# Performance work log

Hardware: AMD Instinct MI355X
Metric: run time of the kernel (lower is better)

Reference implementation:

```python
import jax, jax.numpy as jnp
import numpy as np

P_SIZE = 5
NUM_HEAD = 8
GN_EPS = 1e-5
LRELU_SLOPE = 0.2


def conv1x1(w, x, b=None):
    # w: [out_c, in_c], x: [n, in_c, h, w]
    y = jnp.einsum('oc,nchw->nohw', w, x)
    if b is not None:
        y = y + b[None, :, None, None]
    return y


def bilinear_sample(feat, sx, sy):
    """grid_sample(mode='bilinear', padding_mode='zeros', align_corners=True).
    With align_corners=True the normalize/denormalize round-trip in
    deformation_grid/grid_sample is the identity, so sx,sy are raw pixel coords.
    feat: [n,c,H,W]; sx,sy: [n,P,H,W] -> out [n,c,P,H,W]."""
    n, c, H, W = feat.shape
    x0 = jnp.floor(sx)
    y0 = jnp.floor(sy)
    x1 = x0 + 1.0
    y1 = y0 + 1.0
    wx1 = sx - x0
    wx0 = 1.0 - wx1
    wy1 = sy - y0
    wy0 = 1.0 - wy1
    feat_flat = feat.reshape(n, c, H * W)

    def corner(xi, yi, wgt):
        valid = (xi >= 0) & (xi <= W - 1) & (yi >= 0) & (yi <= H - 1)
        xc = jnp.clip(xi, 0, W - 1).astype(jnp.int32)
        yc = jnp.clip(yi, 0, H - 1).astype(jnp.int32)
        idx = (yc * W + xc).reshape(n, -1)                      # [n, P*H*W]
        g = jnp.take_along_axis(feat_flat, idx[:, None, :], axis=2)  # [n,c,P*H*W]
        g = g.reshape(n, c, xi.shape[1], H, W)                  # [n,c,P,H,W]
        wm = (wgt * valid.astype(feat.dtype))[:, None]          # [n,1,P,H,W]
        return g * wm

    return (corner(x0, y0, wx0 * wy0) + corner(x1, y0, wx1 * wy0)
            + corner(x0, y1, wx0 * wy1) + corner(x1, y1, wx1 * wy1))


def sample_coords(deform_field, p_size):
    # deform_field: [n,2,h,w] -> absolute pixel coords sx, sy: [n, p^2, h, w]
    n, _, h, w = deform_field.shape
    padding = (p_size - 1) // 2
    shift = jnp.arange(p_size, dtype=deform_field.dtype) - padding
    shift_y, shift_x = jnp.meshgrid(shift, shift, indexing='ij')  # [p,p]
    shift_y = shift_y.reshape(-1, 1, 1)  # [p^2,1,1]
    shift_x = shift_x.reshape(-1, 1, 1)
    gy = jnp.arange(h, dtype=deform_field.dtype)[:, None]  # [h,1]
    gx = jnp.arange(w, dtype=deform_field.dtype)[None, :]  # [1,w]
    sx = gx[None] + shift_x + deform_field[:, None, 0]     # [n,p^2,h,w]
    sy = gy[None] + shift_y + deform_field[:, None, 1]
    return sx, sy


def setup_inputs() -> dict:
    key = jax.random.key(0)
    ks = jax.random.split(key, 12)
    n, c, h, w = 2, 128, 96, 96
    hid = 256
    s = 0.05
    return {
        'query': jax.random.normal(ks[0], (n, c, h, w), jnp.float32),
        'key': jax.random.normal(ks[1], (n, c, h, w), jnp.float32),
        'value': jax.random.normal(ks[2], (n, c, h, w), jnp.float32),
        'deform_field': jax.random.normal(ks[3], (n, 2, h, w), jnp.float32) * 2.0,
        'w_q': jax.random.normal(ks[4], (c, c), jnp.float32) * s,
        'w_k': jax.random.normal(ks[5], (c, c), jnp.float32) * s,
        'w_v': jax.random.normal(ks[6], (c, c), jnp.float32) * s,
        'w_fc': jax.random.normal(ks[7], (c, c), jnp.float32) * s,
        'mlp_w1': jax.random.normal(ks[8], (hid, c), jnp.float32) * s,
        'mlp_b1': jnp.zeros((hid,), jnp.float32),
        'mlp_w2': jax.random.normal(ks[9], (c, hid), jnp.float32) * s,
        'mlp_b2': jnp.zeros((c,), jnp.float32),
        'gn_gamma': jnp.ones((c,), jnp.float32),
        'gn_beta': jnp.zeros((c,), jnp.float32),
    }


def reference(query, key, value, deform_field, w_q, w_k, w_v, w_fc,
              mlp_w1, mlp_b1, mlp_w2, mlp_b2, gn_gamma, gn_beta):
    p2 = P_SIZE * P_SIZE
    n, c, h, w = query.shape
    d_k = c // NUM_HEAD

    q = conv1x1(w_q, query)   # [n,c,h,w]
    k = conv1x1(w_k, key)
    v = conv1x1(w_v, value)

    # deformable window sampling of keys/values
    sx, sy = sample_coords(deform_field, P_SIZE)      # [n,p^2,h,w]
    k_s = bilinear_sample(k, sx, sy)                  # [n,c,p^2,h,w]
    v_s = bilinear_sample(v, sx, sy)

    # split heads
    q = q.reshape(n, NUM_HEAD, d_k, h, w)
    k_s = k_s.reshape(n, NUM_HEAD, d_k, p2, h, w)
    v_s = v_s.reshape(n, NUM_HEAD, d_k, p2, h, w)

    scale = 1.0 / jnp.sqrt(jnp.asarray(d_k, q.dtype))
    attn = jnp.einsum('nedyx,nedpyx->neyxp', q * scale, k_s)   # [n,head,h,w,p^2]
    attn = jax.nn.softmax(attn, axis=-1)
    out = jnp.einsum('neyxp,nedpyx->nedyx', attn, v_s)          # [n,head,d_v,h,w]
    out = out.reshape(n, c, h, w)
    out = conv1x1(w_fc, out)

    # conv-MLP residual
    hdn = conv1x1(mlp_w1, out, mlp_b1)
    hdn = jnp.where(hdn >= 0, hdn, LRELU_SLOPE * hdn)
    out = out + conv1x1(mlp_w2, hdn, mlp_b2)

    # GroupNorm(1, feat_dim): normalize over (C,H,W) per sample, per-channel affine
    mean = jnp.mean(out, axis=(1, 2, 3), keepdims=True)
    var = jnp.mean(jnp.square(out - mean), axis=(1, 2, 3), keepdims=True)
    out = (out - mean) * jax.lax.rsqrt(var + GN_EPS)
    out = out * gn_gamma[None, :, None, None] + gn_beta[None, :, None, None]
    return out
```

## Files before the change

### kernel.cpp

```cpp
#include <hip/hip_runtime.h>
#include <cstddef>

constexpr int Cc = 128;
constexpr int Hh = 96;
constexpr int Ww = 96;
constexpr int HW = Hh * Ww;
constexpr int Nn = 2;

typedef __attribute__((ext_vector_type(2))) _Float16 f16x2;
typedef __attribute__((ext_vector_type(4))) _Float16 f16x4;
typedef __attribute__((ext_vector_type(8))) _Float16 f16x8;
typedef __attribute__((ext_vector_type(4))) float f32x4;

__device__ __forceinline__ float fdot2(f16x2 a, f16x2 b, float c) {
#if defined(__has_builtin) && __has_builtin(__builtin_amdgcn_fdot2)
    return __builtin_amdgcn_fdot2(a, b, c, false);
#else
    return (float)a[0] * (float)b[0] + (float)a[1] * (float)b[1] + c;
#endif
}

__global__ void __launch_bounds__(256)
wcvt_k(const float* __restrict__ wq, const float* __restrict__ wk,
       const float* __restrict__ wv, const float* __restrict__ wfc,
       const float* __restrict__ w1, const float* __restrict__ w2,
       _Float16* __restrict__ dst)
{
    const int h0 = (blockIdx.x * 256 + threadIdx.x) * 8;
    const float* src; int off, K;
    if (h0 < 16384)      { src = wq;  off = h0;          K = 128; }
    else if (h0 < 32768) { src = wk;  off = h0 - 16384;  K = 128; }
    else if (h0 < 49152) { src = wv;  off = h0 - 32768;  K = 128; }
    else if (h0 < 65536) { src = wfc; off = h0 - 49152;  K = 128; }
    else if (h0 < 98304) { src = w1;  off = h0 - 65536;  K = 128; }
    else                 { src = w2;  off = h0 - 98304;  K = 256; }
    const int fid  = off >> 3;
    const int lane = fid & 63;
    const int n16  = lane & 15, quad = lane >> 4;
    const int t2   = fid >> 6;
    const int kcN  = K / 32;
    const int kc   = t2 % kcN;
    const int mt   = t2 / kcN;
    const int row  = mt * 16 + n16;
    const int col  = kc * 32 + quad * 8;
    const float* s = src + (size_t)row * K + col;
    const float4 a = *(const float4*)s;
    const float4 b = *(const float4*)(s + 4);
    f16x8 h = {(_Float16)a.x, (_Float16)a.y, (_Float16)a.z, (_Float16)a.w,
               (_Float16)b.x, (_Float16)b.y, (_Float16)b.z, (_Float16)b.w};
    *(f16x8*)&dst[h0] = h;
}

__global__ void __launch_bounds__(128)
qkv_k(const float* __restrict__ Xq, const float* __restrict__ Xk,
      const float* __restrict__ Xv, const _Float16* __restrict__ w16,
      _Float16* __restrict__ q16, _Float16* __restrict__ k16,
      float* __restrict__ v32)
{
    const int t  = blockIdx.y;
    const int p0 = blockIdx.x * 64;
    const int z  = blockIdx.z;
    const float* X = (t == 0) ? Xq : (t == 1) ? Xk : Xv;
    const _Float16* W = w16 + (size_t)t * 16384;

    __shared__ _Float16 xl[128][72];
    const int tid = threadIdx.x;
    {
        const int px4 = (tid & 15) * 4, kg = tid >> 4;
        const float* Xz = X + (size_t)z * Cc * HW + p0 + px4;
#pragma unroll
        for (int kk = 0; kk < 16; ++kk) {
            const int k = kk * 8 + kg;
            float4 a = *(const float4*)&Xz[(size_t)k * HW];
            f16x4 h = {(_Float16)a.x, (_Float16)a.y, (_Float16)a.z, (_Float16)a.w};
            *(f16x4*)&xl[k][px4] = h;
        }
    }
    __syncthreads();

    const int w = tid >> 6, lane = tid & 63;
    const int n16 = lane & 15, quad = lane >> 4;
    const int pw = w * 32;

#pragma unroll
    for (int half = 0; half < 2; ++half) {
        const int oc0 = half * 64;
        f32x4 acc[2][4];
#pragma unroll
        for (int mi = 0; mi < 2; ++mi)
#pragma unroll
            for (int ni = 0; ni < 4; ++ni) acc[mi][ni] = (f32x4)0.f;

#pragma unroll
        for (int kcid = 0; kcid < 4; ++kcid) {
            const int kc = kcid * 32;
            f16x8 A[2], B[4];
#pragma unroll
            for (int mi = 0; mi < 2; ++mi) {
                const int px = pw + mi * 16 + n16;
                f16x8 av;
#pragma unroll
                for (int j = 0; j < 8; ++j) av[j] = xl[kc + quad * 8 + j][px];
                A[mi] = av;
            }
#pragma unroll
            for (int ni = 0; ni < 4; ++ni)
                B[ni] = *(const f16x8*)&W[(((half * 4 + ni) * 4 + kcid) * 64 + lane) * 8];
#pragma unroll
            for (int mi = 0; mi < 2; ++mi)
#pragma unroll
                for (int ni = 0; ni < 4; ++ni)
                    acc[mi][ni] = __builtin_amdgcn_mfma_f32_16x16x32_f16(
                        A[mi], B[ni], acc[mi][ni], 0, 0, 0);
        }

#pragma unroll
        for (int mi = 0; mi < 2; ++mi)
#pragma unroll
            for (int r = 0; r < 4; ++r) {
                const int pix = p0 + pw + mi * 16 + quad * 4 + r;
                const size_t base = ((size_t)z * HW + pix) * Cc + oc0;
                if (t == 0) {
#pragma unroll
                    for (int ni = 0; ni < 4; ++ni)
                        q16[base + ni * 16 + n16] = (_Float16)acc[mi][ni][r];
                } else if (t == 1) {
#pragma unroll
                    for (int ni = 0; ni < 4; ++ni)
                        k16[base + ni * 16 + n16] = (_Float16)acc[mi][ni][r];
                } else {
#pragma unroll
                    for (int ni = 0; ni < 4; ++ni)
                        v32[base + ni * 16 + n16] = acc[mi][ni][r];
                }
            }
    }
}

template<int KT, bool OUTF16, bool BIAS, bool LRELU, bool RESID, bool REDUCE>
__global__ void __launch_bounds__(128)
mg_k(const _Float16* __restrict__ X, const _Float16* __restrict__ Wf,
     const float* __restrict__ bias, const _Float16* __restrict__ resid,
     void* __restrict__ Yv, float* __restrict__ pb, const int Mtot)
{
    constexpr int kcN = KT / 32;
    const int z = blockIdx.z, oc0 = blockIdx.y * 64, p0 = blockIdx.x * 64;
    const int tid = threadIdx.x, w = tid >> 6, lane = tid & 63;
    const int n16 = lane & 15, quad = lane >> 4;
    const _Float16* Xz = X + ((size_t)z * HW + p0 + w * 32) * KT;

    f32x4 acc[2][4];
#pragma unroll
    for (int mi = 0; mi < 2; ++mi)
#pragma unroll
        for (int ni = 0; ni < 4; ++ni) acc[mi][ni] = (f32x4)0.f;

#pragma unroll
    for (int kc = 0; kc < kcN; ++kc) {
        f16x8 A[2], B[4];
#pragma unroll
        for (int mi = 0; mi < 2; ++mi)
            A[mi] = *(const f16x8*)&Xz[(size_t)(mi * 16 + n16) * KT + kc * 32 + quad * 8];
#pragma unroll
        for (int ni = 0; ni < 4; ++ni)
            B[ni] = *(const f16x8*)&Wf[(((blockIdx.y * 4 + ni) * kcN + kc) * 64 + lane) * 8];
#pragma unroll
        for (int mi = 0; mi < 2; ++mi)
#pragma unroll
            for (int ni = 0; ni < 4; ++ni)
                acc[mi][ni] = __builtin_amdgcn_mfma_f32_16x16x32_f16(
                    A[mi], B[ni], acc[mi][ni], 0, 0, 0);
    }

    float bv[4];
#pragma unroll
    for (int ni = 0; ni < 4; ++ni) bv[ni] = BIAS ? bias[oc0 + ni * 16 + n16] : 0.f;

    float lsum = 0.f, lsq = 0.f;
#pragma unroll
    for (int mi = 0; mi < 2; ++mi)
#pragma unroll
        for (int r = 0; r < 4; ++r) {
            const int pix = p0 + w * 32 + mi * 16 + quad * 4 + r;
            const size_t ob = ((size_t)z * HW + pix) * (size_t)Mtot + oc0;
            const size_t rb = ((size_t)z * HW + pix) * 128 + oc0;
#pragma unroll
            for (int ni = 0; ni < 4; ++ni) {
                float tv = acc[mi][ni][r] + bv[ni];
                if (LRELU) tv = tv >= 0.f ? tv : 0.2f * tv;
                if (RESID) tv += (float)resid[rb + ni * 16 + n16];
                if (REDUCE) { lsum += tv; lsq += tv * tv; }
                if (OUTF16) ((_Float16*)Yv)[ob + ni * 16 + n16] = (_Float16)tv;
                else        ((float*)Yv)[ob + ni * 16 + n16] = tv;
            }
        }

    if (REDUCE) {
        __shared__ float red[4];
#pragma unroll
        for (int m = 1; m < 64; m <<= 1) {
            lsum += __shfl_xor(lsum, m, 64);
            lsq  += __shfl_xor(lsq,  m, 64);
        }
        if (lane == 0) { red[w * 2] = lsum; red[w * 2 + 1] = lsq; }
        __syncthreads();
        if (tid == 0) {
            const int bid = (blockIdx.z * gridDim.y + blockIdx.y) * gridDim.x + blockIdx.x;
            pb[bid * 2 + 0] = red[0] + red[2];
            pb[bid * 2 + 1] = red[1] + red[3];
        }
    }
}

__global__ void __launch_bounds__(256)
rsum_k(const float* __restrict__ pb, float* __restrict__ sums, const int nPerZ)
{
    __shared__ float red[8];
    const int z = blockIdx.x, tid = threadIdx.x;
    float s = 0.f, q = 0.f;
    for (int p = tid; p < nPerZ; p += 256) {
        s += pb[(z * nPerZ + p) * 2 + 0];
        q += pb[(z * nPerZ + p) * 2 + 1];
    }
#pragma unroll
    for (int m = 1; m < 64; m <<= 1) {
        s += __shfl_xor(s, m, 64);
        q += __shfl_xor(q, m, 64);
    }
    if ((tid & 63) == 0) { red[(tid >> 6) * 2] = s; red[(tid >> 6) * 2 + 1] = q; }
    __syncthreads();
    if (tid == 0) {
        sums[z * 2 + 0] = red[0] + red[2] + red[4] + red[6];
        sums[z * 2 + 1] = red[1] + red[3] + red[5] + red[7];
    }
}

__global__ void __launch_bounds__(256)
attn_k(const _Float16* __restrict__ q, const _Float16* __restrict__ k,
       const float* __restrict__ v, const float* __restrict__ df,
       _Float16* __restrict__ out)
{
    const int blk = blockIdx.x;
    const int sw = (blk & 7) * (1152 / 8) + (blk >> 3);
    const int wv = sw * 4 + (threadIdx.x >> 6);
    const int lane = threadIdx.x & 63;
    const int gp = wv * 4 + (lane >> 4);
    const int b = gp / HW;
    const int pix = gp - b * HW;
    const int y = pix / Ww, x = pix - y * Ww;
    const int co = (lane & 15) * 8;

    const float dx = df[((size_t)b * 2 + 0) * HW + pix];
    const float dy = df[((size_t)b * 2 + 1) * HW + pix];
    const float flx = floorf(dx), fly = floorf(dy);
    const int bx = x - 2 + (int)flx;
    const int by = y - 2 + (int)fly;
    const float wx1 = dx - flx, wx0 = 1.f - wx1;
    const float wy1 = dy - fly, wy0 = 1.f - wy1;
    const float u00 = wy0 * wx0, u01 = wy0 * wx1, u10 = wy1 * wx0, u11 = wy1 * wx1;
    const float s00 = u00 * 0.25f, s01 = u01 * 0.25f,
                s10 = u10 * 0.25f, s11 = u11 * 0.25f;

    const f16x8 qv8 = *(const f16x8*)&q[((size_t)b * HW + pix) * Cc + co];
    const f16x2 q0 = {qv8[0], qv8[1]}, q1 = {qv8[2], qv8[3]},
                q2 = {qv8[4], qv8[5]}, q3 = {qv8[6], qv8[7]};

    const _Float16* kp = k + ((size_t)b * HW) * Cc + co;
    const float*    vp = v + ((size_t)b * HW) * Cc + co;

    const bool inb = (bx >= 0) & (by >= 0) & (bx <= Ww - 6) & (by <= Hh - 6);
    const int allin = __all(inb);

    float qk[36];
    if (allin) {
        const _Float16* kr = kp + (size_t)(by * Ww + bx) * Cc;
#pragma unroll
        for (int r = 0; r < 6; ++r) {
#pragma unroll
            for (int c = 0; c < 6; ++c) {
                const f16x8 kv = *(const f16x8*)&kr[c * Cc];
                f16x2 k0 = {kv[0], kv[1]}, k1 = {kv[2], kv[3]};
                f16x2 k2 = {kv[4], kv[5]}, k3 = {kv[6], kv[7]};
                float d = fdot2(q0, k0, 0.f);
                d = fdot2(q1, k1, d);
                d = fdot2(q2, k2, d);
                d = fdot2(q3, k3, d);
                qk[r * 6 + c] = d;
            }
            kr += Ww * Cc;
        }
    } else {
#pragma unroll
        for (int r = 0; r < 6; ++r) {
            const int yr = by + r;
            const bool rv = (yr >= 0) & (yr < Hh);
            const int yc = min(max(yr, 0), Hh - 1);
            const _Float16* kr = kp + (size_t)(yc * Ww) * Cc;
#pragma unroll
            for (int c = 0; c < 6; ++c) {
                const int xc = bx + c;
                const bool cv = rv & (xc >= 0) & (xc < Ww);
                const int xcc = min(max(xc, 0), Ww - 1);
                const f16x8 kv = *(const f16x8*)&kr[xcc * Cc];
                f16x2 k0 = {kv[0], kv[1]}, k1 = {kv[2], kv[3]};
                f16x2 k2 = {kv[4], kv[5]}, k3 = {kv[6], kv[7]};
                float d = fdot2(q0, k0, 0.f);
                d = fdot2(q1, k1, d);
                d = fdot2(q2, k2, d);
                d = fdot2(q3, k3, d);
                qk[r * 6 + c] = cv ? d : 0.f;
            }
        }
    }

    float a[25];
#pragma unroll
    for (int py = 0; py < 5; ++py)
#pragma unroll
        for (int px = 0; px < 5; ++px) {
            float tv = s00 * qk[py * 6 + px];
            tv = fmaf(s01, qk[py * 6 + px + 1], tv);
            tv = fmaf(s10, qk[(py + 1) * 6 + px], tv);
            tv = fmaf(s11, qk[(py + 1) * 6 + px + 1], tv);
            a[py * 5 + px] = tv;
        }
#pragma unroll
    for (int i = 0; i < 25; ++i) a[i] += __shfl_xor(a[i], 1, 64);

    float mx = a[0];
#pragma unroll
    for (int i = 1; i < 25; ++i) mx = fmaxf(mx, a[i]);
    float ssum = 0.f;
#pragma unroll
    for (int i = 0; i < 25; ++i) { a[i] = __expf(a[i] - mx); ssum += a[i]; }
    const float inv = 1.f / ssum;

    float wsum[36];
#pragma unroll
    for (int i = 0; i < 36; ++i) wsum[i] = 0.f;
#pragma unroll
    for (int py = 0; py < 5; ++py)
#pragma unroll
        for (int px = 0; px < 5; ++px) {
            const float av = a[py * 5 + px];
            wsum[py * 6 + px]           = fmaf(av, u00, wsum[py * 6 + px]);
            wsum[py * 6 + px + 1]       = fmaf(av, u01, wsum[py * 6 + px + 1]);
            wsum[(py + 1) * 6 + px]     = fmaf(av, u10, wsum[(py + 1) * 6 + px]);
            wsum[(py + 1) * 6 + px + 1] = fmaf(av, u11, wsum[(py + 1) * 6 + px + 1]);
        }

    float o[8] = {0.f, 0.f, 0.f, 0.f, 0.f, 0.f, 0.f, 0.f};
    if (allin) {
        const float* vr = vp + (size_t)(by * Ww + bx) * Cc;
#pragma unroll
        for (int r = 0; r < 6; ++r) {
#pragma unroll
            for (int c = 0; c < 6; ++c) {
                const float4 va = *(const float4*)&vr[c * Cc];
                const float4 vb = *(const float4*)&vr[c * Cc + 4];
                const float wgt = wsum[r * 6 + c];
                o[0] = fmaf(wgt, va.x, o[0]); o[1] = fmaf(wgt, va.y, o[1]);
                o[2] = fmaf(wgt, va.z, o[2]); o[3] = fmaf(wgt, va.w, o[3]);
                o[4] = fmaf(wgt, vb.x, o[4]); o[5] = fmaf(wgt, vb.y, o[5]);
                o[6] = fmaf(wgt, vb.z, o[6]); o[7] = fmaf(wgt, vb.w, o[7]);
            }
            vr += Ww * Cc;
        }
    } else {
#pragma unroll
        for (int r = 0; r < 6; ++r) {
            const int yr = by + r;
            const bool rv = (yr >= 0) & (yr < Hh);
            const int yc = min(max(yr, 0), Hh - 1);
            const float* vr = vp + (size_t)(yc * Ww) * Cc;
#pragma unroll
            for (int c = 0; c < 6; ++c) {
                const int xc = bx + c;
                const bool cv = rv & (xc >= 0) & (xc < Ww);
                const int xcc = min(max(xc, 0), Ww - 1);
                const float4 va = *(const float4*)&vr[xcc * Cc];
                const float4 vb = *(const float4*)&vr[xcc * Cc + 4];
                const float wgt = cv ? wsum[r * 6 + c] : 0.f;
                o[0] = fmaf(wgt, va.x, o[0]); o[1] = fmaf(wgt, va.y, o[1]);
                o[2] = fmaf(wgt, va.z, o[2]); o[3] = fmaf(wgt, va.w, o[3]);
                o[4] = fmaf(wgt, vb.x, o[4]); o[5] = fmaf(wgt, vb.y, o[5]);
                o[6] = fmaf(wgt, vb.z, o[6]); o[7] = fmaf(wgt, vb.w, o[7]);
            }
        }
    }

    f16x8 ov;
#pragma unroll
    for (int j = 0; j < 8; ++j) ov[j] = (_Float16)(o[j] * inv);
    *(f16x8*)&out[((size_t)b * HW + pix) * Cc + co] = ov;
}

__global__ void __launch_bounds__(256)
gn_k(const float* __restrict__ y2, const float* __restrict__ sums,
     const float* __restrict__ gamma, const float* __restrict__ beta,
     float* __restrict__ out)
{
    __shared__ float t[32][68];
    const int z = blockIdx.z, c0 = blockIdx.y * 32, p0 = blockIdx.x * 64;
    const float invN = 1.f / (float)(Cc * HW);
    const float mean = sums[z * 2] * invN;
    const float var  = fmaf(-mean, mean, sums[z * 2 + 1] * invN);
    const float rs = rsqrtf(var + 1e-5f);
    const int tid = threadIdx.x;
    {
        const int px = tid >> 2, cq = tid & 3;
        const float* src = &y2[((size_t)z * HW + p0 + px) * Cc + c0 + cq * 8];
        const float4 a = *(const float4*)src;
        const float4 bq = *(const float4*)(src + 4);
        t[cq * 8 + 0][px] = a.x;  t[cq * 8 + 1][px] = a.y;
        t[cq * 8 + 2][px] = a.z;  t[cq * 8 + 3][px] = a.w;
        t[cq * 8 + 4][px] = bq.x; t[cq * 8 + 5][px] = bq.y;
        t[cq * 8 + 6][px] = bq.z; t[cq * 8 + 7][px] = bq.w;
    }
    __syncthreads();
    {
        const int c = tid >> 3, pq = tid & 7;
        const float g = gamma[c0 + c] * rs, be = beta[c0 + c];
        float4 o1, o2;
        o1.x = fmaf(t[c][pq * 8 + 0] - mean, g, be);
        o1.y = fmaf(t[c][pq * 8 + 1] - mean, g, be);
        o1.z = fmaf(t[c][pq * 8 + 2] - mean, g, be);
        o1.w = fmaf(t[c][pq * 8 + 3] - mean, g, be);
        o2.x = fmaf(t[c][pq * 8 + 4] - mean, g, be);
        o2.y = fmaf(t[c][pq * 8 + 5] - mean, g, be);
        o2.z = fmaf(t[c][pq * 8 + 6] - mean, g, be);
        o2.w = fmaf(t[c][pq * 8 + 7] - mean, g, be);
        float* dst = &out[((size_t)z * Cc + c0 + c) * HW + p0 + pq * 8];
        *(float4*)dst = o1;
        *(float4*)(dst + 4) = o2;
    }
}

extern "C" void kernel_launch(void* const* d_in, const int* in_sizes, int n_in,
                              void* d_out, int out_size, void* d_ws, size_t ws_size,
                              hipStream_t stream)
{
    const float* query  = (const float*)d_in[0];
    const float* key    = (const float*)d_in[1];
    const float* value  = (const float*)d_in[2];
    const float* deform = (const float*)d_in[3];
    const float* w_q    = (const float*)d_in[4];
    const float* w_k    = (const float*)d_in[5];
    const float* w_v    = (const float*)d_in[6];
    const float* w_fc   = (const float*)d_in[7];
    const float* mlp_w1 = (const float*)d_in[8];
    const float* mlp_b1 = (const float*)d_in[9];
    const float* mlp_w2 = (const float*)d_in[10];
    const float* mlp_b2 = (const float*)d_in[11];
    const float* gn_g   = (const float*)d_in[12];
    const float* gn_b   = (const float*)d_in[13];
    float* out = (float*)d_out;

    char* wsb = (char*)d_ws;
    _Float16* w16 = (_Float16*)wsb;
    float* sums = (float*)(wsb + 262144);
    float* pb   = (float*)(wsb + 266240);
    _Float16* T = (_Float16*)(wsb + 524288);
    const size_t S16 = (size_t)Nn * HW * Cc;
    _Float16* q16  = T;
    _Float16* k16  = T + S16;
    float*    v32  = (float*)(T + 2 * S16);
    _Float16* at16 = T + 4 * S16;
    _Float16* y1   = T + 5 * S16;
    _Float16* hb   = T;
    float*    y2   = v32;

    wcvt_k<<<dim3(64), dim3(256), 0, stream>>>(
        w_q, w_k, w_v, w_fc, mlp_w1, mlp_w2, w16);

    qkv_k<<<dim3(HW / 64, 3, Nn), dim3(128), 0, stream>>>(
        query, key, value, w16, q16, k16, v32);

    attn_k<<<dim3(Nn * HW / 16), dim3(256), 0, stream>>>(
        q16, k16, v32, deform, at16);

    mg_k<128, true, false, false, false, false>
        <<<dim3(HW / 64, 2, Nn), dim3(128), 0, stream>>>(
        at16, w16 + 49152, nullptr, nullptr, y1, nullptr, 128);

    mg_k<128, true, true, true, false, false>
        <<<dim3(HW / 64, 4, Nn), dim3(128), 0, stream>>>(
        y1, w16 + 65536, mlp_b1, nullptr, hb, nullptr, 256);

    mg_k<256, false, true, false, true, true>
        <<<dim3(HW / 64, 2, Nn), dim3(128), 0, stream>>>(
        hb, w16 + 98304, mlp_b2, y1, y2, pb, 128);

    rsum_k<<<dim3(Nn), dim3(256), 0, stream>>>(pb, sums, 288);

    gn_k<<<dim3(HW / 64, Cc / 32, Nn), dim3(256), 0, stream>>>(
        y2, sums, gn_g, gn_b, out);
}
```

Baseline: 161.1 us.

## Store V in fp16, separate bilinear weight spreading, fold GN reduction into normalize kernel

V projection output is now stored as fp16 instead of fp32, halving the bytes gathered per sample in the attention kernel. The spreading of softmax weights onto the 6x6 bilinear footprint is rewritten as separable row-then-column passes, which uses fewer FMAs. The separate partial-sum reduction kernel is removed: every GroupNorm block now re-reduces the 288 partials per sample itself, saving a launch at the cost of redundant work. Storing V in fp16 lowers precision.

```diff
diff --git a/kernel.cpp b/kernel.cpp
--- a/kernel.cpp
+++ b/kernel.cpp
@@ -55,12 +55,13 @@
 qkv_k(const float* __restrict__ Xq, const float* __restrict__ Xk,
       const float* __restrict__ Xv, const _Float16* __restrict__ w16,
       _Float16* __restrict__ q16, _Float16* __restrict__ k16,
-      float* __restrict__ v32)
+      _Float16* __restrict__ v16)
 {
     const int t  = blockIdx.y;
     const int p0 = blockIdx.x * 64;
     const int z  = blockIdx.z;
     const float* X = (t == 0) ? Xq : (t == 1) ? Xk : Xv;
+    _Float16* Y    = (t == 0) ? q16 : (t == 1) ? k16 : v16;
     const _Float16* W = w16 + (size_t)t * 16384;
 
     __shared__ _Float16 xl[128][72];
@@ -120,19 +121,9 @@
             for (int r = 0; r < 4; ++r) {
                 const int pix = p0 + pw + mi * 16 + quad * 4 + r;
                 const size_t base = ((size_t)z * HW + pix) * Cc + oc0;
-                if (t == 0) {
-#pragma unroll
-                    for (int ni = 0; ni < 4; ++ni)
-                        q16[base + ni * 16 + n16] = (_Float16)acc[mi][ni][r];
-                } else if (t == 1) {
-#pragma unroll
-                    for (int ni = 0; ni < 4; ++ni)
-                        k16[base + ni * 16 + n16] = (_Float16)acc[mi][ni][r];
-                } else {
-#pragma unroll
-                    for (int ni = 0; ni < 4; ++ni)
-                        v32[base + ni * 16 + n16] = acc[mi][ni][r];
-                }
+#pragma unroll
+                for (int ni = 0; ni < 4; ++ni)
+                    Y[base + ni * 16 + n16] = (_Float16)acc[mi][ni][r];
             }
     }
 }
@@ -213,31 +204,8 @@
 }
 
 __global__ void __launch_bounds__(256)
-rsum_k(const float* __restrict__ pb, float* __restrict__ sums, const int nPerZ)
-{
-    __shared__ float red[8];
-    const int z = blockIdx.x, tid = threadIdx.x;
-    float s = 0.f, q = 0.f;
-    for (int p = tid; p < nPerZ; p += 256) {
-        s += pb[(z * nPerZ + p) * 2 + 0];
-        q += pb[(z * nPerZ + p) * 2 + 1];
-    }
-#pragma unroll
-    for (int m = 1; m < 64; m <<= 1) {
-        s += __shfl_xor(s, m, 64);
-        q += __shfl_xor(q, m, 64);
-    }
-    if ((tid & 63) == 0) { red[(tid >> 6) * 2] = s; red[(tid >> 6) * 2 + 1] = q; }
-    __syncthreads();
-    if (tid == 0) {
-        sums[z * 2 + 0] = red[0] + red[2] + red[4] + red[6];
-        sums[z * 2 + 1] = red[1] + red[3] + red[5] + red[7];
-    }
-}
-
-__global__ void __launch_bounds__(256)
 attn_k(const _Float16* __restrict__ q, const _Float16* __restrict__ k,
-       const float* __restrict__ v, const float* __restrict__ df,
+       const _Float16* __restrict__ v, const float* __restrict__ df,
        _Float16* __restrict__ out)
 {
     const int blk = blockIdx.x;
@@ -266,7 +234,7 @@
                 q2 = {qv8[4], qv8[5]}, q3 = {qv8[6], qv8[7]};
 
     const _Float16* kp = k + ((size_t)b * HW) * Cc + co;
-    const float*    vp = v + ((size_t)b * HW) * Cc + co;
+    const _Float16* vp = v + ((size_t)b * HW) * Cc + co;
 
     const bool inb = (bx >= 0) & (by >= 0) & (bx <= Ww - 6) & (by <= Hh - 6);
     const int allin = __all(inb);
@@ -335,34 +303,39 @@
     for (int i = 0; i < 25; ++i) { a[i] = __expf(a[i] - mx); ssum += a[i]; }
     const float inv = 1.f / ssum;
 
+    float tmp[6][5];
+#pragma unroll
+    for (int r = 0; r < 6; ++r)
+#pragma unroll
+        for (int px = 0; px < 5; ++px) {
+            float tv = 0.f;
+            if (r < 5)  tv = a[r * 5 + px] * wy0;
+            if (r >= 1) tv = fmaf(a[(r - 1) * 5 + px], wy1, tv);
+            tmp[r][px] = tv;
+        }
     float wsum[36];
 #pragma unroll
-    for (int i = 0; i < 36; ++i) wsum[i] = 0.f;
-#pragma unroll
-    for (int py = 0; py < 5; ++py)
-#pragma unroll
-        for (int px = 0; px < 5; ++px) {
-            const float av = a[py * 5 + px];
-            wsum[py * 6 + px]           = fmaf(av, u00, wsum[py * 6 + px]);
-            wsum[py * 6 + px + 1]       = fmaf(av, u01, wsum[py * 6 + px + 1]);
-            wsum[(py + 1) * 6 + px]     = fmaf(av, u10, wsum[(py + 1) * 6 + px]);
-            wsum[(py + 1) * 6 + px + 1] = fmaf(av, u11, wsum[(py + 1) * 6 + px + 1]);
+    for (int r = 0; r < 6; ++r)
+#pragma unroll
+        for (int c = 0; c < 6; ++c) {
+            float tv = 0.f;
+            if (c < 5)  tv = tmp[r][c] * wx0;
+            if (c >= 1) tv = fmaf(tmp[r][c - 1], wx1, tv);
+            wsum[r * 6 + c] = tv;
         }
 
     float o[8] = {0.f, 0.f, 0.f, 0.f, 0.f, 0.f, 0.f, 0.f};
     if (allin) {
-        const float* vr = vp + (size_t)(by * Ww + bx) * Cc;
+        const _Float16* vr = vp + (size_t)(by * Ww + bx) * Cc;
 #pragma unroll
         for (int r = 0; r < 6; ++r) {
 #pragma unroll
             for (int c = 0; c < 6; ++c) {
-                const float4 va = *(const float4*)&vr[c * Cc];
-                const float4 vb = *(const float4*)&vr[c * Cc + 4];
+                const f16x8 vv = *(const f16x8*)&vr[c * Cc];
                 const float wgt = wsum[r * 6 + c];
-                o[0] = fmaf(wgt, va.x, o[0]); o[1] = fmaf(wgt, va.y, o[1]);
-                o[2] = fmaf(wgt, va.z, o[2]); o[3] = fmaf(wgt, va.w, o[3]);
-                o[4] = fmaf(wgt, vb.x, o[4]); o[5] = fmaf(wgt, vb.y, o[5]);
-                o[6] = fmaf(wgt, vb.z, o[6]); o[7] = fmaf(wgt, vb.w, o[7]);
+#pragma unroll
+                for (int j = 0; j < 8; ++j)
+                    o[j] = fmaf(wgt, (float)vv[j], o[j]);
             }
             vr += Ww * Cc;
         }
@@ -372,19 +345,17 @@
             const int yr = by + r;
             const bool rv = (yr >= 0) & (yr < Hh);
             const int yc = min(max(yr, 0), Hh - 1);
-            const float* vr = vp + (size_t)(yc * Ww) * Cc;
+            const _Float16* vr = vp + (size_t)(yc * Ww) * Cc;
 #pragma unroll
             for (int c = 0; c < 6; ++c) {
                 const int xc = bx + c;
                 const bool cv = rv & (xc >= 0) & (xc < Ww);
                 const int xcc = min(max(xc, 0), Ww - 1);
-                const float4 va = *(const float4*)&vr[xcc * Cc];
-                const float4 vb = *(const float4*)&vr[xcc * Cc + 4];
+                const f16x8 vv = *(const f16x8*)&vr[xcc * Cc];
                 const float wgt = cv ? wsum[r * 6 + c] : 0.f;
-                o[0] = fmaf(wgt, va.x, o[0]); o[1] = fmaf(wgt, va.y, o[1]);
-                o[2] = fmaf(wgt, va.z, o[2]); o[3] = fmaf(wgt, va.w, o[3]);
-                o[4] = fmaf(wgt, vb.x, o[4]); o[5] = fmaf(wgt, vb.y, o[5]);
-                o[6] = fmaf(wgt, vb.z, o[6]); o[7] = fmaf(wgt, vb.w, o[7]);
+#pragma unroll
+                for (int j = 0; j < 8; ++j)
+                    o[j] = fmaf(wgt, (float)vv[j], o[j]);
             }
         }
     }
@@ -396,17 +367,32 @@
 }
 
 __global__ void __launch_bounds__(256)
-gn_k(const float* __restrict__ y2, const float* __restrict__ sums,
+gn_k(const float* __restrict__ y2, const float* __restrict__ pb,
      const float* __restrict__ gamma, const float* __restrict__ beta,
-     float* __restrict__ out)
+     float* __restrict__ out, const int nPerZ)
 {
     __shared__ float t[32][68];
+    __shared__ float redm[8];
+    __shared__ float stats[2];
     const int z = blockIdx.z, c0 = blockIdx.y * 32, p0 = blockIdx.x * 64;
-    const float invN = 1.f / (float)(Cc * HW);
-    const float mean = sums[z * 2] * invN;
-    const float var  = fmaf(-mean, mean, sums[z * 2 + 1] * invN);
-    const float rs = rsqrtf(var + 1e-5f);
     const int tid = threadIdx.x;
+
+    {
+        float s = 0.f, qq = 0.f;
+        for (int p = tid; p < nPerZ; p += 256) {
+            s  += pb[(z * nPerZ + p) * 2 + 0];
+            qq += pb[(z * nPerZ + p) * 2 + 1];
+        }
+#pragma unroll
+        for (int m = 1; m < 64; m <<= 1) {
+            s  += __shfl_xor(s,  m, 64);
+            qq += __shfl_xor(qq, m, 64);
+        }
+        if ((tid & 63) == 0) {
+            redm[(tid >> 6) * 2]     = s;
+            redm[(tid >> 6) * 2 + 1] = qq;
+        }
+    }
     {
         const int px = tid >> 2, cq = tid & 3;
         const float* src = &y2[((size_t)z * HW + p0 + px) * Cc + c0 + cq * 8];
@@ -418,7 +404,18 @@
         t[cq * 8 + 6][px] = bq.z; t[cq * 8 + 7][px] = bq.w;
     }
     __syncthreads();
+    if (tid == 0) {
+        const float invN = 1.f / (float)(Cc * HW);
+        const float S = redm[0] + redm[2] + redm[4] + redm[6];
+        const float Q = redm[1] + redm[3] + redm[5] + redm[7];
+        const float mean = S * invN;
+        const float var  = fmaf(-mean, mean, Q * invN);
+        stats[0] = mean;
+        stats[1] = rsqrtf(var + 1e-5f);
+    }
+    __syncthreads();
     {
+        const float mean = stats[0], rs = stats[1];
         const int c = tid >> 3, pq = tid & 7;
         const float g = gamma[c0 + c] * rs, be = beta[c0 + c];
         float4 o1, o2;
@@ -458,26 +455,25 @@
 
     char* wsb = (char*)d_ws;
     _Float16* w16 = (_Float16*)wsb;
-    float* sums = (float*)(wsb + 262144);
-    float* pb   = (float*)(wsb + 266240);
+    float* pb   = (float*)(wsb + 262144);
     _Float16* T = (_Float16*)(wsb + 524288);
     const size_t S16 = (size_t)Nn * HW * Cc;
     _Float16* q16  = T;
     _Float16* k16  = T + S16;
-    float*    v32  = (float*)(T + 2 * S16);
-    _Float16* at16 = T + 4 * S16;
-    _Float16* y1   = T + 5 * S16;
+    _Float16* v16  = T + 2 * S16;
+    _Float16* at16 = T + 3 * S16;
+    _Float16* y1   = T + 4 * S16;
     _Float16* hb   = T;
-    float*    y2   = v32;
+    float*    y2   = (float*)(T + 2 * S16);
 
     wcvt_k<<<dim3(64), dim3(256), 0, stream>>>(
         w_q, w_k, w_v, w_fc, mlp_w1, mlp_w2, w16);
 
     qkv_k<<<dim3(HW / 64, 3, Nn), dim3(128), 0, stream>>>(
-        query, key, value, w16, q16, k16, v32);
+        query, key, value, w16, q16, k16, v16);
 
     attn_k<<<dim3(Nn * HW / 16), dim3(256), 0, stream>>>(
-        q16, k16, v32, deform, at16);
+        q16, k16, v16, deform, at16);
 
     mg_k<128, true, false, false, false, false>
         <<<dim3(HW / 64, 2, Nn), dim3(128), 0, stream>>>(
@@ -491,8 +487,6 @@
         <<<dim3(HW / 64, 2, Nn), dim3(128), 0, stream>>>(
         hb, w16 + 98304, mlp_b2, y1, y2, pb, 128);
 
-    rsum_k<<<dim3(Nn), dim3(256), 0, stream>>>(pb, sums, 288);
-
     gn_k<<<dim3(HW / 64, Cc / 32, Nn), dim3(256), 0, stream>>>(
-        y2, sums, gn_g, gn_b, out);
-}
+        y2, pb, gn_g, gn_b, out, 288);
+}
```

Result: faster. 156.8 us (-2.7%).
